# Kernel tuning notes

Measured on AMD Instinct MI355X. Metric: run time of the kernel, lower is better.

## Reference

```python
import jax, jax.numpy as jnp
import numpy as np

LOGZERO = -1.0e10


def setup_inputs() -> dict:
    bs, xmax, vocab, ymax = 16, 512, 4000, 64
    key = jax.random.key(0)
    k1, k2, k3, k4 = jax.random.split(key, 4)
    ctc_out = jax.nn.log_softmax(jax.random.normal(k1, (bs, xmax, vocab), jnp.float32), axis=-1)
    src_size = jax.random.randint(k2, (bs,), xmax // 2, xmax + 1, dtype=jnp.int32)
    src_mask = jnp.arange(xmax)[None, None, :] < src_size[:, None, None]  # [bs,1,xmax] bool
    ys = jax.random.randint(k3, (bs, ymax), 1, vocab, dtype=jnp.int32)     # non-blank labels
    ylens = jax.random.randint(k4, (bs,), ymax // 2, ymax + 1, dtype=jnp.int32)
    return {"ctc_out": ctc_out, "src_mask": src_mask, "src_size": src_size,
            "ys": ys, "ylens": ylens, "blank": 0}


def reference(ctc_out, src_mask, src_size, ys, ylens, blank):
    bs, xmax, vocab = ctc_out.shape
    ymax = ys.shape[1]
    L = 2 * ymax + 1  # CTC path length (blank-interleaved)

    # mask invalid frames, time-major: [xmax, bs, vocab]
    lp = jnp.where(src_mask[:, 0, :, None], ctc_out, LOGZERO).transpose(1, 0, 2)

    # blank-interleaved path: [bs, L]
    path = jnp.full((bs, L), blank, dtype=ys.dtype).at[:, 1::2].set(ys)
    path_lens = 2 * ylens + 1

    # per-path-state log-probs: [xmax, bs, L]
    lpp = jnp.take_along_axis(lp, jnp.broadcast_to(path[None], (xmax, bs, L)), axis=2)

    same_transition = path[:, :-2] == path[:, 2:]           # [bs, L-2]
    index_fix = jnp.arange(L)
    outside = index_fix[None, :] >= path_lens[:, None]       # [bs, L]
    alpha0 = jnp.full((bs, L), LOGZERO, jnp.float32).at[:, 0].set(0.0)

    neg1 = jnp.full((bs, 1), LOGZERO, jnp.float32)
    neg2 = jnp.full((bs, 2), LOGZERO, jnp.float32)

    def dp_step(alpha, lp_t):
        m0 = alpha
        m1 = jnp.concatenate([neg1, alpha[:, :-1]], axis=1)
        m2 = jnp.concatenate([neg2, jnp.where(same_transition, LOGZERO, alpha[:, :-2])], axis=1)
        mat = jnp.stack([m0, m1, m2])                        # [3, bs, L]
        max_prob = jnp.where(outside, LOGZERO, mat.max(axis=0))
        bp_t = index_fix[None, :] - mat.argmax(axis=0)       # predecessor path index
        alpha_new = max_prob + lp_t
        return alpha_new, (bp_t, alpha_new)

    _, (bp, alpha_stack) = jax.lax.scan(dp_step, alpha0, lpp)  # [xmax,bs,L] each

    # alpha at t = src_size[b] for each batch element
    alpha_bt = alpha_stack.transpose(1, 0, 2)                # [bs, xmax, L]
    alpha_final = jnp.take_along_axis(alpha_bt, (src_size - 1)[:, None, None], axis=1)[:, 0, :]
    s1 = jnp.take_along_axis(alpha_final, (path_lens - 1)[:, None], axis=1)[:, 0]
    s2 = jnp.take_along_axis(alpha_final, (path_lens - 2)[:, None], axis=1)[:, 0]
    init_state = jnp.where(s1 > s2, path_lens - 1, path_lens - 2).astype(jnp.int32)
    score = jnp.maximum(s1, s2)  # Viterbi alignment score (diagnostic/diff output)

    # vectorized backtrace: reverse scan over time, per-batch state
    ts = jnp.arange(xmax - 1, -1, -1)

    def bt_step(cur, xs):
        bp_t, t = xs  # bp_t: [bs, L]
        cur_t = jnp.where(t == src_size - 1, init_state, cur)
        out_t = jnp.where(t <= src_size - 1, cur_t, 0)
        nxt = jnp.where((t >= 1) & (t <= src_size - 1),
                        jnp.take_along_axis(bp_t, cur_t[:, None], axis=1)[:, 0].astype(jnp.int32),
                        cur_t)
        return nxt, out_t

    _, outs = jax.lax.scan(bt_step, jnp.zeros((bs,), jnp.int32), (bp[::-1], ts))
    aligned_states = outs[::-1].T                            # [bs, xmax]

    # map path indices back to labels, then collapse repeats to blank(=0)
    aligned_seq = jnp.take_along_axis(path, aligned_states, axis=1)
    shift = jnp.concatenate([jnp.zeros((bs, 1), aligned_seq.dtype), aligned_seq[:, :-1]], 1)
    aligned_seq = jnp.where(aligned_seq == shift, 0, aligned_seq)
    aligned_seq_shift = jnp.concatenate([jnp.zeros((bs, 1), aligned_seq.dtype), aligned_seq[:, :-1]], 1)

    # trigger mask: [bs, ymax+1, xmax]
    trig = jnp.cumsum((aligned_seq_shift != blank).astype(jnp.int32), axis=1)
    trigger_mask = trig[:, None, :] == jnp.arange(ymax + 1)[None, :, None]
    last = trigger_mask[:, -1, :] & src_mask[:, 0, :]
    last = last.at[jnp.arange(bs), src_size - 1].set(True)
    trigger_mask = trigger_mask.at[:, -1, :].set(last)

    return aligned_seq, trigger_mask, ylens + 1, score
```

## Files before the change

### kernel.cpp

```cpp
#include <hip/hip_runtime.h>

#define LOGZERO (-1.0e10f)

constexpr int BS    = 16;
constexpr int XMAX  = 512;
constexpr int VOCAB = 4000;
constexpr int YMAX  = 64;
constexpr int PF    = 8;
constexpr int TCH   = 8;
constexpr int GRP   = 16;
constexpr int NG    = XMAX / GRP;
constexpr int CH    = 16;
constexpr int CL    = 32;

constexpr size_t AS_OFF = 0;
constexpr size_t TM_OFF = (size_t)BS * XMAX;
constexpr size_t YL_OFF = TM_OFF + (size_t)BS * (YMAX + 1) * XMAX;
constexpr size_t SC_OFF = YL_OFF + BS;
constexpr size_t WS_STRIDE_F = 8192;

__device__ __forceinline__ float dpp_shr1_f(float x, float fill) {
    return __int_as_float(__builtin_amdgcn_update_dpp(
        __float_as_int(fill), __float_as_int(x), 0x138 , 0xF, 0xF, false));
}
__device__ __forceinline__ int dpp_shr1_i(int x, int fill) {
    return __builtin_amdgcn_update_dpp(fill, x, 0x138, 0xF, 0xF, false);
}
__device__ __forceinline__ int dpp_id_i(int x) {
    return __builtin_amdgcn_update_dpp(0, x, 0xE4 , 0xF, 0xF, false);
}

__global__ __launch_bounds__(64)
void gather_kernel(const float* __restrict__ ctc,
                   const int* __restrict__ ys,
                   const int* __restrict__ blank_p,
                   float* __restrict__ out)
{
    const int tc   = blockIdx.x;
    const int b    = blockIdx.y;
    const int lane = threadIdx.x;

    const int blank = blank_p[0];
    const int ysv   = ys[b * YMAX + lane];

    const float* base = ctc + ((size_t)b * XMAX + (size_t)tc * TCH) * VOCAB;

    float v[TCH];
    #pragma unroll
    for (int j = 0; j < TCH; ++j)
        v[j] = base[(size_t)j * VOCAB + ysv];
    const float bl = base[(size_t)(lane & (TCH - 1)) * VOCAB + blank];

    float* lpp = out + TM_OFF + (size_t)b * (YMAX + 1) * XMAX + (size_t)tc * TCH * 65;
    #pragma unroll
    for (int j = 0; j < TCH; ++j)
        lpp[(size_t)j * 65 + lane] = v[j];
    if (lane < TCH)
        lpp[(size_t)lane * 65 + 64] = bl;
}

__global__ __launch_bounds__(256)
void dp_loop_kernel(const int* __restrict__ src_size,
                    const int* __restrict__ ys,
                    const int* __restrict__ ylens,
                    const float* __restrict__ out_ro,
                    float* __restrict__ out,
                    float* __restrict__ ws)
{
    const int b    = blockIdx.x;
    const int tid  = threadIdx.x;
    const int lane = tid & 63;

    const int ss    = src_size[b];
    const int ylen  = ylens[b];
    const int plen  = 2 * ylen + 1;
    const int ssm1  = ss - 1;
    const int g0    = (ss + GRP - 1) >> 4;

    __shared__ __align__(16) float lppL[(XMAX + PF) * 65];

    const float* gbase = out_ro + TM_OFF + (size_t)b * (YMAX + 1) * XMAX;
    float*       wsb   = ws + (size_t)b * WS_STRIDE_F;

    {
        const float4* src = (const float4*)gbase;
        float4* dst = (float4*)lppL;
        #pragma unroll 4
        for (int i = tid; i < XMAX * 65 / 4; i += 256)
            dst[i] = src[i];
    }
    __syncthreads();

    if (tid < 64) {
        const int  ysv    = ys[b * YMAX + lane];
        const int  ysPrev = dpp_shr1_i(ysv, -1);
        const bool sameO  = (ysv == ysPrev);

        uint2* dgl = (uint2*)wsb + lane;

        float rO[PF], rB[PF];
        #pragma unroll
        for (int k = 0; k < PF; ++k) {
            rO[k] = lppL[k * 65 + lane];
            rB[k] = lppL[k * 65 + 64];
        }

        float aE = (lane == 0) ? 0.0f : LOGZERO;
        float aO = LOGZERO;
        float aX = LOGZERO;
        float fE = LOGZERO, fO = LOGZERO, fX = LOGZERO;
        int offO = PF * 65 + lane, offB = PF * 65 + 64;

        const int SS16 = g0 << 4;
        for (int tb = 0; tb < SS16; tb += GRP) {
            unsigned w0 = 0u, w1 = 0u;
            #pragma unroll
            for (int j = 0; j < GRP; ++j) {
                const int K = j & (PF - 1);
                const float lpO = rO[K], lpB = rB[K];
                rO[K] = lppL[offO]; rB[K] = lppL[offB]; offO += 65; offB += 65;
                const float prevO = dpp_shr1_f(aO, LOGZERO);
                const float m2v   = sameO ? LOGZERO : prevO;
                const float b01   = fmaxf(aO, aE);
                int oIdx = (aE > aO) ? 1 : 0;
                oIdx = (m2v > b01) ? 2 : oIdx;
                w0 |= (prevO > aE) ? (1u << j) : 0u;
                w0 |= (aO > aX)   ? (1u << (16 + j)) : 0u;
                w1 |= ((unsigned)oIdx) << (2 * j);
                aX = fmaxf(aX, aO) + lpB;
                aO = fmaxf(b01, m2v) + lpO;
                aE = fmaxf(aE, prevO) + lpB;
                const bool cap = (tb + j == ssm1);
                fE = cap ? aE : fE;
                fO = cap ? aO : fO;
                fX = cap ? aX : fX;
            }
            uint2 sv;
            sv.x = (unsigned)dpp_id_i((int)w0);
            sv.y = (unsigned)dpp_id_i((int)w1);
            *dgl = sv;
            dgl += 64;
        }

        const float s1 = (ylen == YMAX) ? __shfl(fX, 63) : __shfl(fE, ylen);
        const float s2 = __shfl(fO, ylen - 1);
        if (lane == 0) {
            out[SC_OFF + b] = fmaxf(s1, s2);
            out[YL_OFF + b] = (float)(ylen + 1);
            ((int*)wsb)[4096] = (s1 > s2) ? (plen - 1) : (plen - 2);
        }
    } else {
        uint2 z; z.x = 0u; z.y = 0u;
        uint2* dz = (uint2*)wsb;
        for (int i = g0 * 64 + (tid - 64); i < NG * 64; i += 192)
            dz[i] = z;
    }
}

__device__ __forceinline__ int jstep(const uint2* __restrict__ DL,
                                     int T, int s, int ist, int ssm1)
{
    const int g  = T >> 4;
    const int j  = T & 15;
    const int ct = (T == ssm1) ? ist : s;
    const int l  = (ct >= 128) ? 63 : (ct >> 1);
    const uint2 w = DL[g * 64 + l];
    const int ce = (int)((w.x >> j) & 1u);
    const int co = (int)((w.y >> (2 * j)) & 3u);
    const int cx = (int)((w.x >> (16 + j)) & 1u);
    int code = (ct & 1) ? co : ce;
    code = (ct == 128) ? cx : code;
    code = (T >= 1 && T <= ssm1) ? code : 0;
    return ct - code;
}

__global__ __launch_bounds__(256)
void btfused_kernel(const int* __restrict__ src_size,
                    const int* __restrict__ ys,
                    const int* __restrict__ blank_p,
                    float* __restrict__ out,
                    const float* __restrict__ ws)
{
    const int b    = blockIdx.x;
    const int tid  = threadIdx.x;
    const int lane = tid & 63;

    const int blank = blank_p[0];
    const int ss    = src_size[b];

    __shared__ uint2 DL[NG * 64];
    __shared__ int   E[CH][130];
    __shared__ int   CE[CH];
    __shared__ int   states[XMAX];
    __shared__ int   trig[XMAX];
    __shared__ int   ysL[YMAX];
    __shared__ int   istS;

    const float* wsb   = ws + (size_t)b * WS_STRIDE_F;
    float*       gbase = out + TM_OFF + (size_t)b * (YMAX + 1) * XMAX;

    {
        const float4* src = (const float4*)wsb;
        float4* dst = (float4*)DL;
        for (int i = tid; i < NG * 64 * 8 / 16; i += 256)
            dst[i] = src[i];
    }
    if (tid < YMAX) ysL[tid] = ys[b * YMAX + tid];
    if (tid == 0)   istS = ((const int*)wsb)[4096];
    __syncthreads();

    const int ist  = istS;
    const int ssm1 = ss - 1;

    constexpr int TK4 = (CH * 130) / 4;
    for (int p = tid; p < TK4; p += 256) {
        const int tA = p, tB = p + TK4, tC = p + 2 * TK4, tD = p + 3 * TK4;
        const int cA = tA / 130, eA = tA - cA * 130;
        const int cB = tB / 130, eB = tB - cB * 130;
        const int cC = tC / 130, eC = tC - cC * 130;
        const int cD = tD / 130, eD = tD - cD * 130;
        int sA = min(eA, 128), sB = min(eB, 128), sC = min(eC, 128), sD = min(eD, 128);
        #pragma unroll 4
        for (int j = 0; j < CL; ++j) {
            sA = jstep(DL, cA * CL + (CL - 1) - j, sA, ist, ssm1);
            sB = jstep(DL, cB * CL + (CL - 1) - j, sB, ist, ssm1);
            sC = jstep(DL, cC * CL + (CL - 1) - j, sC, ist, ssm1);
            sD = jstep(DL, cD * CL + (CL - 1) - j, sD, ist, ssm1);
        }
        E[cA][eA] = sA; E[cB][eB] = sB; E[cC][eC] = sC; E[cD][eD] = sD;
    }
    __syncthreads();

    if (tid == 0) {
        int cur = 0;
        for (int c = CH - 1; c >= 0; --c) {
            CE[c] = cur;
            cur = E[c][cur];
        }
    }
    __syncthreads();

    if (tid < CH) {
        int s = CE[tid];
        for (int j = 0; j < CL; ++j) {
            const int T  = tid * CL + (CL - 1) - j;
            const int ct = (T == ssm1) ? ist : s;
            states[T] = (T <= ssm1) ? ct : 0;
            s = jstep(DL, T, s, ist, ssm1);
        }
    }
    __syncthreads();

    if (tid < 64) {
        const int t8 = lane * 8;
        int sq[8];
        #pragma unroll
        for (int j = 0; j < 8; ++j) {
            const int st = states[t8 + j];
            sq[j] = (st & 1) ? ysL[st >> 1] : blank;
        }
        int prevLast = __shfl_up(sq[7], 1);
        if (lane == 0) prevLast = 0;

        int cl[8];
        #pragma unroll
        for (int j = 0; j < 8; ++j) {
            const int pv = j ? sq[j - 1] : prevLast;
            cl[j] = (sq[j] == pv) ? 0 : sq[j];
        }

        {
            float* as = out + AS_OFF + (size_t)b * XMAX + t8;
            float4 o0, o1;
            o0.x = (float)cl[0]; o0.y = (float)cl[1]; o0.z = (float)cl[2]; o0.w = (float)cl[3];
            o1.x = (float)cl[4]; o1.y = (float)cl[5]; o1.z = (float)cl[6]; o1.w = (float)cl[7];
            *(float4*)as = o0; *((float4*)as + 1) = o1;
        }

        int cnt = 0;
        #pragma unroll
        for (int j = 0; j < 8; ++j) cnt += (cl[j] != blank);
        int x = cnt;
        #pragma unroll
        for (int d = 1; d < 64; d <<= 1) {
            const int y = __shfl_up(x, d);
            if (lane >= d) x += y;
        }
        int run = x - cnt + ((0 != blank) ? 1 : 0);
        #pragma unroll
        for (int j = 0; j < 8; ++j) {
            trig[t8 + j] = run;
            run += (cl[j] != blank);
        }
    }
    __syncthreads();

    float* tm = gbase;
    for (int i4 = tid * 4; i4 < (YMAX + 1) * XMAX; i4 += 256 * 4) {
        const int y  = i4 >> 9;
        const int t0 = i4 & (XMAX - 1);
        const int4 tg4 = *(const int4*)&trig[t0];
        float4 v;
        if (y == YMAX) {
            v.x = ((tg4.x == YMAX && (t0 + 0) < ss) || (t0 + 0) == ss - 1) ? 1.0f : 0.0f;
            v.y = ((tg4.y == YMAX && (t0 + 1) < ss) || (t0 + 1) == ss - 1) ? 1.0f : 0.0f;
            v.z = ((tg4.z == YMAX && (t0 + 2) < ss) || (t0 + 2) == ss - 1) ? 1.0f : 0.0f;
            v.w = ((tg4.w == YMAX && (t0 + 3) < ss) || (t0 + 3) == ss - 1) ? 1.0f : 0.0f;
        } else {
            v.x = (tg4.x == y) ? 1.0f : 0.0f;
            v.y = (tg4.y == y) ? 1.0f : 0.0f;
            v.z = (tg4.z == y) ? 1.0f : 0.0f;
            v.w = (tg4.w == y) ? 1.0f : 0.0f;
        }
        *(float4*)(tm + i4) = v;
    }
}

extern "C" void kernel_launch(void* const* d_in, const int* in_sizes, int n_in,
                              void* d_out, int out_size, void* d_ws, size_t ws_size,
                              hipStream_t stream) {
    (void)in_sizes; (void)n_in; (void)ws_size; (void)out_size;
    const float* ctc      = (const float*)d_in[0];
    const int*   src_size = (const int*)d_in[2];
    const int*   ys       = (const int*)d_in[3];
    const int*   ylens    = (const int*)d_in[4];
    const int*   blank    = (const int*)d_in[5];
    float*       out      = (float*)d_out;
    float*       ws       = (float*)d_ws;

    dim3 g1(XMAX / TCH, BS);
    gather_kernel<<<g1, 64, 0, stream>>>(ctc, ys, blank, out);
    dp_loop_kernel<<<BS, 256, 0, stream>>>(src_size, ys, ylens, out, out, ws);
    btfused_kernel<<<BS, 256, 0, stream>>>(src_size, ys, blank, out, ws);
}
```

Baseline: 86.64 us.

## Fuse DP forward pass and backtrace into one kernel with shared decision bits

Merges the forward Viterbi DP kernel and the backtrace/trigger kernel into a single per-batch kernel. Decision bitmasks now stay in shared memory instead of going through a global workspace, and shared memory is aliased between the log-prob staging buffer and the backtrace arrays. The DP loop now stops exactly at src_size, with a partial tail group, so the final alphas come straight from the loop rather than from per-step capture selects. This removes one launch and a global round trip, at the cost of a large shared-memory footprint per block.

Result: faster. 79.35 us (-8.4%).

```diff
diff --git a/kernel.cpp b/kernel.cpp
--- a/kernel.cpp
+++ b/kernel.cpp
@@ -17,7 +17,6 @@
 constexpr size_t TM_OFF = (size_t)BS * XMAX;
 constexpr size_t YL_OFF = TM_OFF + (size_t)BS * (YMAX + 1) * XMAX;
 constexpr size_t SC_OFF = YL_OFF + BS;
-constexpr size_t WS_STRIDE_F = 8192;
 
 __device__ __forceinline__ float dpp_shr1_f(float x, float fill) {
     return __int_as_float(__builtin_amdgcn_update_dpp(
@@ -25,9 +24,6 @@
 }
 __device__ __forceinline__ int dpp_shr1_i(int x, int fill) {
     return __builtin_amdgcn_update_dpp(fill, x, 0x138, 0xF, 0xF, false);
-}
-__device__ __forceinline__ int dpp_id_i(int x) {
-    return __builtin_amdgcn_update_dpp(0, x, 0xE4 , 0xF, 0xF, false);
 }
 
 __global__ __launch_bounds__(64)
@@ -59,106 +55,24 @@
         lpp[(size_t)lane * 65 + 64] = bl;
 }
 
-__global__ __launch_bounds__(256)
-void dp_loop_kernel(const int* __restrict__ src_size,
-                    const int* __restrict__ ys,
-                    const int* __restrict__ ylens,
-                    const float* __restrict__ out_ro,
-                    float* __restrict__ out,
-                    float* __restrict__ ws)
-{
-    const int b    = blockIdx.x;
-    const int tid  = threadIdx.x;
-    const int lane = tid & 63;
-
-    const int ss    = src_size[b];
-    const int ylen  = ylens[b];
-    const int plen  = 2 * ylen + 1;
-    const int ssm1  = ss - 1;
-    const int g0    = (ss + GRP - 1) >> 4;
-
-    __shared__ __align__(16) float lppL[(XMAX + PF) * 65];
-
-    const float* gbase = out_ro + TM_OFF + (size_t)b * (YMAX + 1) * XMAX;
-    float*       wsb   = ws + (size_t)b * WS_STRIDE_F;
-
-    {
-        const float4* src = (const float4*)gbase;
-        float4* dst = (float4*)lppL;
-        #pragma unroll 4
-        for (int i = tid; i < XMAX * 65 / 4; i += 256)
-            dst[i] = src[i];
-    }
-    __syncthreads();
-
-    if (tid < 64) {
-        const int  ysv    = ys[b * YMAX + lane];
-        const int  ysPrev = dpp_shr1_i(ysv, -1);
-        const bool sameO  = (ysv == ysPrev);
-
-        uint2* dgl = (uint2*)wsb + lane;
-
-        float rO[PF], rB[PF];
-        #pragma unroll
-        for (int k = 0; k < PF; ++k) {
-            rO[k] = lppL[k * 65 + lane];
-            rB[k] = lppL[k * 65 + 64];
-        }
-
-        float aE = (lane == 0) ? 0.0f : LOGZERO;
-        float aO = LOGZERO;
-        float aX = LOGZERO;
-        float fE = LOGZERO, fO = LOGZERO, fX = LOGZERO;
-        int offO = PF * 65 + lane, offB = PF * 65 + 64;
-
-        const int SS16 = g0 << 4;
-        for (int tb = 0; tb < SS16; tb += GRP) {
-            unsigned w0 = 0u, w1 = 0u;
-            #pragma unroll
-            for (int j = 0; j < GRP; ++j) {
-                const int K = j & (PF - 1);
-                const float lpO = rO[K], lpB = rB[K];
-                rO[K] = lppL[offO]; rB[K] = lppL[offB]; offO += 65; offB += 65;
-                const float prevO = dpp_shr1_f(aO, LOGZERO);
-                const float m2v   = sameO ? LOGZERO : prevO;
-                const float b01   = fmaxf(aO, aE);
-                int oIdx = (aE > aO) ? 1 : 0;
-                oIdx = (m2v > b01) ? 2 : oIdx;
-                w0 |= (prevO > aE) ? (1u << j) : 0u;
-                w0 |= (aO > aX)   ? (1u << (16 + j)) : 0u;
-                w1 |= ((unsigned)oIdx) << (2 * j);
-                aX = fmaxf(aX, aO) + lpB;
-                aO = fmaxf(b01, m2v) + lpO;
-                aE = fmaxf(aE, prevO) + lpB;
-                const bool cap = (tb + j == ssm1);
-                fE = cap ? aE : fE;
-                fO = cap ? aO : fO;
-                fX = cap ? aX : fX;
-            }
-            uint2 sv;
-            sv.x = (unsigned)dpp_id_i((int)w0);
-            sv.y = (unsigned)dpp_id_i((int)w1);
-            *dgl = sv;
-            dgl += 64;
-        }
-
-        const float s1 = (ylen == YMAX) ? __shfl(fX, 63) : __shfl(fE, ylen);
-        const float s2 = __shfl(fO, ylen - 1);
-        if (lane == 0) {
-            out[SC_OFF + b] = fmaxf(s1, s2);
-            out[YL_OFF + b] = (float)(ylen + 1);
-            ((int*)wsb)[4096] = (s1 > s2) ? (plen - 1) : (plen - 2);
-        }
-    } else {
-        uint2 z; z.x = 0u; z.y = 0u;
-        uint2* dz = (uint2*)wsb;
-        for (int i = g0 * 64 + (tid - 64); i < NG * 64; i += 192)
-            dz[i] = z;
-    }
-}
-
-__device__ __forceinline__ int jstep(const uint2* __restrict__ DL,
-                                     int T, int s, int ist, int ssm1)
+#define DP_STEP(K, J)                                                          \
+{                                                                              \
+    const float lpO = rO[K], lpB = rB[K];                                      \
+    rO[K] = lppL[offO]; rB[K] = lppL[offB]; offO += 65; offB += 65;            \
+    const float prevO = dpp_shr1_f(aO, LOGZERO);                               \
+    const float m2v   = sameO ? LOGZERO : prevO;                               \
+    const float b01   = fmaxf(aO, aE);                                         \
+    int oIdx = (aE > aO) ? 1 : 0;                                              \
+    oIdx = (m2v > b01) ? 2 : oIdx;                                             \
+    w0 |= (prevO > aE) ? (1u << (J)) : 0u;                                     \
+    w0 |= (aO > aX)    ? (1u << (16 + (J))) : 0u;                              \
+    w1 |= ((unsigned)oIdx) << (2 * (J));                                       \
+    aX = fmaxf(aX, aO) + lpB;                                                  \
+    aO = fmaxf(b01, m2v) + lpO;                                                \
+    aE = fmaxf(aE, prevO) + lpB;                                               \
+}
+
+__device__ __forceinline__ int jstep(const uint2* DL, int T, int s, int ist, int ssm1)
 {
     const int g  = T >> 4;
     const int j  = T & 15;
@@ -175,11 +89,11 @@
 }
 
 __global__ __launch_bounds__(256)
-void btfused_kernel(const int* __restrict__ src_size,
-                    const int* __restrict__ ys,
-                    const int* __restrict__ blank_p,
-                    float* __restrict__ out,
-                    const float* __restrict__ ws)
+void fused_kernel(const int* __restrict__ src_size,
+                  const int* __restrict__ ys,
+                  const int* __restrict__ ylens,
+                  const int* __restrict__ blank_p,
+                  float* __restrict__ out)
 {
     const int b    = blockIdx.x;
     const int tid  = threadIdx.x;
@@ -187,30 +101,87 @@
 
     const int blank = blank_p[0];
     const int ss    = src_size[b];
-
-    __shared__ uint2 DL[NG * 64];
-    __shared__ int   E[CH][130];
-    __shared__ int   CE[CH];
-    __shared__ int   states[XMAX];
-    __shared__ int   trig[XMAX];
-    __shared__ int   ysL[YMAX];
-    __shared__ int   istS;
-
-    const float* wsb   = ws + (size_t)b * WS_STRIDE_F;
-    float*       gbase = out + TM_OFF + (size_t)b * (YMAX + 1) * XMAX;
+    const int ylen  = ylens[b];
+    const int plen  = 2 * ylen + 1;
+    const int ssm1  = ss - 1;
+    const int gAll  = (ss + GRP - 1) >> 4;
+
+    __shared__ __align__(16) char  smem[(XMAX + PF) * 65 * 4];
+    __shared__ __align__(16) uint2 DLs[NG * 64];
+    __shared__ int CE[CH];
+    __shared__ int ysL[YMAX];
+    __shared__ int istS;
+
+    float* lppL   = (float*)smem;
+    int*   E      = (int*)smem;
+    int*   states = (int*)(smem + CH * 130 * 4);
+    int*   trig   = (int*)(smem + CH * 130 * 4 + XMAX * 4);
+
+    float* gbase = out + TM_OFF + (size_t)b * (YMAX + 1) * XMAX;
 
     {
-        const float4* src = (const float4*)wsb;
-        float4* dst = (float4*)DL;
-        for (int i = tid; i < NG * 64 * 8 / 16; i += 256)
+        const float4* src = (const float4*)gbase;
+        float4* dst = (float4*)lppL;
+        #pragma unroll 4
+        for (int i = tid; i < XMAX * 65 / 4; i += 256)
             dst[i] = src[i];
     }
     if (tid < YMAX) ysL[tid] = ys[b * YMAX + tid];
-    if (tid == 0)   istS = ((const int*)wsb)[4096];
-    __syncthreads();
-
-    const int ist  = istS;
-    const int ssm1 = ss - 1;
+    __syncthreads();
+
+    if (tid < 64) {
+        const int  ysv    = ys[b * YMAX + lane];
+        const int  ysPrev = dpp_shr1_i(ysv, -1);
+        const bool sameO  = (ysv == ysPrev);
+
+        float rO[PF], rB[PF];
+        #pragma unroll
+        for (int k = 0; k < PF; ++k) {
+            rO[k] = lppL[k * 65 + lane];
+            rB[k] = lppL[k * 65 + 64];
+        }
+
+        float aE = (lane == 0) ? 0.0f : LOGZERO;
+        float aO = LOGZERO;
+        float aX = LOGZERO;
+        int offO = PF * 65 + lane, offB = PF * 65 + 64;
+        int t = 0, g = 0;
+
+        while (t + GRP <= ss) {
+            unsigned w0 = 0u, w1 = 0u;
+            #pragma unroll
+            for (int j = 0; j < GRP; ++j) { DP_STEP(j & (PF - 1), j) }
+            t += GRP;
+            uint2 sv; sv.x = w0; sv.y = w1;
+            DLs[g * 64 + lane] = sv;
+            ++g;
+        }
+        const int rem = ss - t;
+        if (rem > 0) {
+            unsigned w0 = 0u, w1 = 0u;
+            #pragma unroll
+            for (int j = 0; j < GRP; ++j) {
+                if (j < rem) { DP_STEP(j & (PF - 1), j) }
+            }
+            uint2 sv; sv.x = w0; sv.y = w1;
+            DLs[g * 64 + lane] = sv;
+        }
+
+        const float s1 = (ylen == YMAX) ? __shfl(aX, 63) : __shfl(aE, ylen);
+        const float s2 = __shfl(aO, ylen - 1);
+        if (lane == 0) {
+            out[SC_OFF + b] = fmaxf(s1, s2);
+            out[YL_OFF + b] = (float)(ylen + 1);
+            istS = (s1 > s2) ? (plen - 1) : (plen - 2);
+        }
+    } else {
+        uint2 z; z.x = 0u; z.y = 0u;
+        for (int i = gAll * 64 + (tid - 64); i < NG * 64; i += 192)
+            DLs[i] = z;
+    }
+    __syncthreads();
+
+    const int ist = istS;
 
     constexpr int TK4 = (CH * 130) / 4;
     for (int p = tid; p < TK4; p += 256) {
@@ -222,12 +193,13 @@
         int sA = min(eA, 128), sB = min(eB, 128), sC = min(eC, 128), sD = min(eD, 128);
         #pragma unroll 4
         for (int j = 0; j < CL; ++j) {
-            sA = jstep(DL, cA * CL + (CL - 1) - j, sA, ist, ssm1);
-            sB = jstep(DL, cB * CL + (CL - 1) - j, sB, ist, ssm1);
-            sC = jstep(DL, cC * CL + (CL - 1) - j, sC, ist, ssm1);
-            sD = jstep(DL, cD * CL + (CL - 1) - j, sD, ist, ssm1);
-        }
-        E[cA][eA] = sA; E[cB][eB] = sB; E[cC][eC] = sC; E[cD][eD] = sD;
+            sA = jstep(DLs, cA * CL + (CL - 1) - j, sA, ist, ssm1);
+            sB = jstep(DLs, cB * CL + (CL - 1) - j, sB, ist, ssm1);
+            sC = jstep(DLs, cC * CL + (CL - 1) - j, sC, ist, ssm1);
+            sD = jstep(DLs, cD * CL + (CL - 1) - j, sD, ist, ssm1);
+        }
+        E[cA * 130 + eA] = sA; E[cB * 130 + eB] = sB;
+        E[cC * 130 + eC] = sC; E[cD * 130 + eD] = sD;
     }
     __syncthreads();
 
@@ -235,7 +207,7 @@
         int cur = 0;
         for (int c = CH - 1; c >= 0; --c) {
             CE[c] = cur;
-            cur = E[c][cur];
+            cur = E[c * 130 + cur];
         }
     }
     __syncthreads();
@@ -246,7 +218,7 @@
             const int T  = tid * CL + (CL - 1) - j;
             const int ct = (T == ssm1) ? ist : s;
             states[T] = (T <= ssm1) ? ct : 0;
-            s = jstep(DL, T, s, ist, ssm1);
+            s = jstep(DLs, T, s, ist, ssm1);
         }
     }
     __syncthreads();
@@ -319,17 +291,15 @@
 extern "C" void kernel_launch(void* const* d_in, const int* in_sizes, int n_in,
                               void* d_out, int out_size, void* d_ws, size_t ws_size,
                               hipStream_t stream) {
-    (void)in_sizes; (void)n_in; (void)ws_size; (void)out_size;
+    (void)in_sizes; (void)n_in; (void)d_ws; (void)ws_size; (void)out_size;
     const float* ctc      = (const float*)d_in[0];
     const int*   src_size = (const int*)d_in[2];
     const int*   ys       = (const int*)d_in[3];
     const int*   ylens    = (const int*)d_in[4];
     const int*   blank    = (const int*)d_in[5];
     float*       out      = (float*)d_out;
-    float*       ws       = (float*)d_ws;
 
     dim3 g1(XMAX / TCH, BS);
     gather_kernel<<<g1, 64, 0, stream>>>(ctc, ys, blank, out);
-    dp_loop_kernel<<<BS, 256, 0, stream>>>(src_size, ys, ylens, out, out, ws);
-    btfused_kernel<<<BS, 256, 0, stream>>>(src_size, ys, blank, out, ws);
-}
+    fused_kernel<<<BS, 256, 0, stream>>>(src_size, ys, ylens, blank, out);
+}
```
